# Optimization experiments

Hardware: AMD Instinct MI355X
Metric: run time of the kernel (lower is better)

## Reference

```python
import jax, jax.numpy as jnp
import numpy as np

N = 50000      # nodes (single ntype 'author')
E = 800000     # edges per relation (avg degree 16)
IN = 256       # in_size
H = 4          # num_heads
D = 64         # out_size per head
NEG_SLOPE = 0.2  # DGL GATConv default LeakyReLU slope


def setup_inputs() -> dict:
    key = jax.random.key(0)
    ks = jax.random.split(key, 16)
    s = 1.0 / np.sqrt(IN)
    inp = {
        "h":   jax.random.normal(ks[0], (N, IN), jnp.float32),
        "Wg1": jax.random.normal(ks[1], (H * D, IN), jnp.float32) * s,
        "al1": jax.random.normal(ks[2], (H, D), jnp.float32) * s,
        "ar1": jax.random.normal(ks[3], (H, D), jnp.float32) * s,
        "b1":  jax.random.normal(ks[4], (H * D,), jnp.float32) * 0.01,
        "Wg2": jax.random.normal(ks[5], (H * D, IN), jnp.float32) * s,
        "al2": jax.random.normal(ks[6], (H, D), jnp.float32) * s,
        "ar2": jax.random.normal(ks[7], (H, D), jnp.float32) * s,
        "b2":  jax.random.normal(ks[8], (H * D,), jnp.float32) * 0.01,
        "Wfc": jax.random.normal(ks[9], (H * D, 2 * H * D), jnp.float32) * (1.0 / np.sqrt(2 * H * D)),
        "bfc": jax.random.normal(ks[10], (H * D,), jnp.float32) * 0.01,
        "src1": jax.random.randint(ks[11], (E,), 0, N, jnp.int32),
        "dst1": jax.random.randint(ks[12], (E,), 0, N, jnp.int32),
        "src2": jax.random.randint(ks[13], (E,), 0, N, jnp.int32),
        "dst2": jax.random.randint(ks[14], (E,), 0, N, jnp.int32),
    }
    return inp


def _gat(h, W, al, ar, b, src, dst):
    # DGL GATConv: linear proj -> per-head attn logits -> edge softmax over dst -> scatter-sum
    feat = (h @ W.T).reshape(N, H, D)                       # [N,H,D]
    el = jnp.sum(feat * al, axis=-1)                        # [N,H]
    er = jnp.sum(feat * ar, axis=-1)                        # [N,H]
    e = jax.nn.leaky_relu(el[src] + er[dst], NEG_SLOPE)     # [E,H]
    emax = jax.ops.segment_max(e, dst, num_segments=N)      # [N,H]
    ex = jnp.exp(e - emax[dst])                             # [E,H]
    denom = jax.ops.segment_sum(ex, dst, num_segments=N)    # [N,H]
    alpha = ex / denom[dst]                                 # [E,H]
    msg = feat[src] * alpha[..., None]                      # [E,H,D]
    out = jax.ops.segment_sum(msg, dst, num_segments=N)     # [N,H,D]
    return out.reshape(N, H * D) + b                        # flatten(1) + bias


def reference(h, Wg1, al1, ar1, b1, Wg2, al2, ar2, b2, Wfc, bfc,
              src1, dst1, src2, dst2):
    o1 = _gat(h, Wg1, al1, ar1, b1, src1, dst1)             # metapath 1
    o2 = _gat(h, Wg2, al2, ar2, b2, src2, dst2)             # metapath 2
    sem = jnp.concatenate([o1, o2], axis=1)                 # [N, 2*H*D]
    return sem @ Wfc.T + bfc                                # [N, H*D]
```

## Files before the change

kernel.cpp:

```cpp
#include <hip/hip_runtime.h>
#include <hip/hip_bf16.h>
#include <cfloat>

#define NN 50000
#define EE 800000
#define CAP 64

typedef short bf16x8 __attribute__((ext_vector_type(8)));
typedef float f32x4 __attribute__((ext_vector_type(4)));

__device__ __forceinline__ float leaky(float x) { return x > 0.f ? x : 0.2f * x; }

__device__ __forceinline__ ushort f2b(float x) {
  union { float f; uint u; } v; v.f = x;
  uint r = (v.u + 0x7fffu + ((v.u >> 16) & 1u)) >> 16;
  return (ushort)r;
}
__device__ __forceinline__ float b2f(ushort u) {
  union { uint u; float f; } v; v.u = ((uint)u) << 16; return v.f;
}

#define NH4   (NN * 256 / 4)
#define NW14  (256 * 256 / 4)
#define NW24  (256 * 256 / 4)
#define NWF4  (256 * 512 / 4)
#define NC4   (2 * NN / 4)
#define B0 NH4
#define B1 (B0 + NW14)
#define B2 (B1 + NW24)
#define B3 (B2 + NWF4)
#define B4 (B3 + NC4)

__global__ __launch_bounds__(256) void fused_prep(const float* __restrict__ h,
                                                  const float* __restrict__ Wg1,
                                                  const float* __restrict__ Wg2,
                                                  const float* __restrict__ Wfc,
                                                  ushort* __restrict__ hb,
                                                  ushort* __restrict__ wg1b,
                                                  ushort* __restrict__ wg2b,
                                                  ushort* __restrict__ wfcb,
                                                  int* __restrict__ cursor) {
  int idx = blockIdx.x * blockDim.x + threadIdx.x;
  const float* in;
  ushort* outp;
  int off;
  if (idx < B0) { in = h; outp = hb; off = idx; }
  else if (idx < B1) { in = Wg1; outp = wg1b; off = idx - B0; }
  else if (idx < B2) { in = Wg2; outp = wg2b; off = idx - B1; }
  else if (idx < B3) { in = Wfc; outp = wfcb; off = idx - B2; }
  else if (idx < B4) {
    int4 z = make_int4(0, 0, 0, 0);
    *(int4*)(cursor + (idx - B3) * 4) = z;
    return;
  } else return;
  float4 v = *(const float4*)(in + (size_t)off * 4);
  ushort4 o;
  o.x = f2b(v.x); o.y = f2b(v.y); o.z = f2b(v.z); o.w = f2b(v.w);
  *(ushort4*)(outp + (size_t)off * 4) = o;
}

#define NPROJX ((NN + 127) / 128)
#define PROJ_BLOCKS (NPROJX * 2 * 2)
#define SCAT_BLOCKS (2 * EE / 8 / 256 + 1)
#define MERGED_GRID (SCAT_BLOCKS * 3)

__global__ __launch_bounds__(256) void proj_scatter(const ushort* __restrict__ A,
                                                    const ushort* __restrict__ B1w,
                                                    const ushort* __restrict__ B2w,
                                                    ushort* __restrict__ C, int M,
                                                    const int* __restrict__ src1,
                                                    const int* __restrict__ dst1,
                                                    const int* __restrict__ src2,
                                                    const int* __restrict__ dst2,
                                                    int* __restrict__ cursor,
                                                    ushort* __restrict__ esrc) {
  int r3 = blockIdx.x % 3;
  int g3 = blockIdx.x / 3;
  if (r3 == 0) {
    int g = g3 * 256 + threadIdx.x;
    const int EG = EE / 8;
    if (g >= 2 * EG) return;
    const int* src;
    const int* dst;
    int off, nodeoff;
    if (g < EG) { src = src1; dst = dst1; off = g * 8; nodeoff = 0; }
    else { src = src2; dst = dst2; off = (g - EG) * 8; nodeoff = NN; }
    int4 da = *(const int4*)(dst + off);
    int4 db = *(const int4*)(dst + off + 4);
    int4 sa = *(const int4*)(src + off);
    int4 sb = *(const int4*)(src + off + 4);
    int n0 = nodeoff + da.x, n1 = nodeoff + da.y, n2 = nodeoff + da.z, n3 = nodeoff + da.w;
    int n4 = nodeoff + db.x, n5 = nodeoff + db.y, n6 = nodeoff + db.z, n7 = nodeoff + db.w;
    int p0 = atomicAdd(&cursor[n0], 1);
    int p1 = atomicAdd(&cursor[n1], 1);
    int p2 = atomicAdd(&cursor[n2], 1);
    int p3 = atomicAdd(&cursor[n3], 1);
    int p4 = atomicAdd(&cursor[n4], 1);
    int p5 = atomicAdd(&cursor[n5], 1);
    int p6 = atomicAdd(&cursor[n6], 1);
    int p7 = atomicAdd(&cursor[n7], 1);
    if (p0 < CAP) esrc[(size_t)n0 * CAP + p0] = (ushort)sa.x;
    if (p1 < CAP) esrc[(size_t)n1 * CAP + p1] = (ushort)sa.y;
    if (p2 < CAP) esrc[(size_t)n2 * CAP + p2] = (ushort)sa.z;
    if (p3 < CAP) esrc[(size_t)n3 * CAP + p3] = (ushort)sa.w;
    if (p4 < CAP) esrc[(size_t)n4 * CAP + p4] = (ushort)sb.x;
    if (p5 < CAP) esrc[(size_t)n5 * CAP + p5] = (ushort)sb.y;
    if (p6 < CAP) esrc[(size_t)n6 * CAP + p6] = (ushort)sb.z;
    if (p7 < CAP) esrc[(size_t)n7 * CAP + p7] = (ushort)sb.w;
    return;
  }
  __shared__ __align__(16) ushort As[128][40];
  __shared__ __align__(16) ushort Bs[128][40];
  int pb = 2 * g3 + (r3 - 1);
  if (pb >= PROJ_BLOCKS) return;
  int bz = pb / (NPROJX * 2);
  int rem = pb - bz * (NPROJX * 2);
  int by = rem / NPROJX;
  int bx = rem - by * NPROJX;
  const ushort* B = bz ? B2w : B1w;
  ushort* Cz = C + (size_t)bz * NN * 256;
  int t = threadIdx.x;
  int wave = t >> 6, lane = t & 63;
  int m0 = bx * 128, n0 = by * 128;
  int wm = (wave >> 1) * 64, wn = (wave & 1) * 64;
  int quad = lane >> 4, l15 = lane & 15;
  f32x4 acc[4][4] = {};
  for (int k0 = 0; k0 < 256; k0 += 32) {
#pragma unroll
    for (int i = 0; i < 2; ++i) {
      int c = t + 256 * i;
      int row = c >> 2, ko = (c & 3) * 8;
      uint4 av = make_uint4(0u, 0u, 0u, 0u);
      int gr = m0 + row;
      if (gr < M) av = *(const uint4*)(A + (size_t)gr * 256 + k0 + ko);
      *(uint4*)&As[row][ko] = av;
      uint4 bv = *(const uint4*)(B + (size_t)(n0 + row) * 256 + k0 + ko);
      *(uint4*)&Bs[row][ko] = bv;
    }
    __syncthreads();
    bf16x8 af[4], bf[4];
#pragma unroll
    for (int mt = 0; mt < 4; ++mt) af[mt] = *(const bf16x8*)&As[wm + mt * 16 + l15][quad * 8];
#pragma unroll
    for (int nt = 0; nt < 4; ++nt) bf[nt] = *(const bf16x8*)&Bs[wn + nt * 16 + l15][quad * 8];
#pragma unroll
    for (int mt = 0; mt < 4; ++mt)
#pragma unroll
      for (int nt = 0; nt < 4; ++nt)
        acc[mt][nt] = __builtin_amdgcn_mfma_f32_16x16x32_bf16(af[mt], bf[nt], acc[mt][nt], 0, 0, 0);
    __syncthreads();
  }
#pragma unroll
  for (int mt = 0; mt < 4; ++mt)
#pragma unroll
    for (int r = 0; r < 4; ++r) {
      int row = m0 + wm + mt * 16 + quad * 4 + r;
      if (row < M) {
#pragma unroll
        for (int nt = 0; nt < 4; ++nt)
          Cz[(size_t)row * 256 + n0 + wn + nt * 16 + l15] = f2b(acc[mt][nt][r]);
      }
    }
}

__global__ __launch_bounds__(256) void mfma_fc(const ushort* __restrict__ A0,
                                               const ushort* __restrict__ A1,
                                               const ushort* __restrict__ B,
                                               const float* __restrict__ bias,
                                               float* __restrict__ C, int M) {
  __shared__ __align__(16) ushort As[128][40];
  __shared__ __align__(16) ushort Bs[128][40];
  int t = threadIdx.x;
  int wave = t >> 6, lane = t & 63;
  int m0 = blockIdx.x * 128, n0 = blockIdx.y * 128;
  int wm = (wave >> 1) * 64, wn = (wave & 1) * 64;
  int quad = lane >> 4, l15 = lane & 15;
  f32x4 acc[4][4] = {};
  for (int k0 = 0; k0 < 512; k0 += 32) {
    const ushort* Asrc = (k0 < 256) ? A0 : A1;
    int ka = k0 & 255;
#pragma unroll
    for (int i = 0; i < 2; ++i) {
      int c = t + 256 * i;
      int row = c >> 2, ko = (c & 3) * 8;
      uint4 av = make_uint4(0u, 0u, 0u, 0u);
      int gr = m0 + row;
      if (gr < M) av = *(const uint4*)(Asrc + (size_t)gr * 256 + ka + ko);
      *(uint4*)&As[row][ko] = av;
      uint4 bv = *(const uint4*)(B + (size_t)(n0 + row) * 512 + k0 + ko);
      *(uint4*)&Bs[row][ko] = bv;
    }
    __syncthreads();
    bf16x8 af[4], bf[4];
#pragma unroll
    for (int mt = 0; mt < 4; ++mt) af[mt] = *(const bf16x8*)&As[wm + mt * 16 + l15][quad * 8];
#pragma unroll
    for (int nt = 0; nt < 4; ++nt) bf[nt] = *(const bf16x8*)&Bs[wn + nt * 16 + l15][quad * 8];
#pragma unroll
    for (int mt = 0; mt < 4; ++mt)
#pragma unroll
      for (int nt = 0; nt < 4; ++nt)
        acc[mt][nt] = __builtin_amdgcn_mfma_f32_16x16x32_bf16(af[mt], bf[nt], acc[mt][nt], 0, 0, 0);
    __syncthreads();
  }
#pragma unroll
  for (int mt = 0; mt < 4; ++mt)
#pragma unroll
    for (int r = 0; r < 4; ++r) {
      int row = m0 + wm + mt * 16 + quad * 4 + r;
      if (row < M) {
#pragma unroll
        for (int nt = 0; nt < 4; ++nt) {
          int col = n0 + wn + nt * 16 + l15;
          C[(size_t)row * 256 + col] = acc[mt][nt][r] + bias[col];
        }
      }
    }
}

__global__ __launch_bounds__(256) void eler_kernel(const ushort* __restrict__ feat,
                                                   const float* __restrict__ al1,
                                                   const float* __restrict__ ar1,
                                                   const float* __restrict__ al2,
                                                   const float* __restrict__ ar2,
                                                   float* __restrict__ el,
                                                   float* __restrict__ er) {
  int n = blockIdx.x, c = threadIdx.x;
  const float* al = (n < NN) ? al1 : al2;
  const float* ar = (n < NN) ? ar1 : ar2;
  float v = b2f(feat[(size_t)n * 256 + c]);
  float pl = v * al[c], pr = v * ar[c];
#pragma unroll
  for (int o = 32; o > 0; o >>= 1) {
    pl += __shfl_xor(pl, o);
    pr += __shfl_xor(pr, o);
  }
  if ((c & 63) == 0) {
    el[n * 4 + (c >> 6)] = pl;
    er[n * 4 + (c >> 6)] = pr;
  }
}

__global__ __launch_bounds__(256) void gat_accum(const ushort* __restrict__ feat,
                                                 const float* __restrict__ el,
                                                 const float* __restrict__ er,
                                                 const ushort* __restrict__ esrc,
                                                 const int* __restrict__ deg,
                                                 const float* __restrict__ b1,
                                                 const float* __restrict__ b2,
                                                 ushort* __restrict__ o1,
                                                 ushort* __restrict__ o2) {
  int n = blockIdx.x * 4 + (threadIdx.x >> 6);
  if (n >= 2 * NN) return;
  int lane = threadIdx.x & 63;
  int h = lane >> 4;
  int d = min(deg[n], CAP);
  int nodeoff = (n < NN) ? 0 : NN;
  const ushort* lst = esrc + (size_t)n * CAP;
  float erh = er[n * 4 + h];
  float dsum = 0.f;
  float4 acc0 = make_float4(0.f, 0.f, 0.f, 0.f);
  float4 acc1 = make_float4(0.f, 0.f, 0.f, 0.f);
  float4 acc2 = make_float4(0.f, 0.f, 0.f, 0.f);
  float4 acc3 = make_float4(0.f, 0.f, 0.f, 0.f);
  int i = 0;
  for (; i + 4 <= d; i += 4) {
    ushort4 ss = *(const ushort4*)(lst + i);
    int s0 = ss.x + nodeoff, s1 = ss.y + nodeoff, s2 = ss.z + nodeoff, s3 = ss.w + nodeoff;
    ushort4 f0 = *(const ushort4*)(feat + (size_t)s0 * 256 + lane * 4);
    ushort4 f1 = *(const ushort4*)(feat + (size_t)s1 * 256 + lane * 4);
    ushort4 f2 = *(const ushort4*)(feat + (size_t)s2 * 256 + lane * 4);
    ushort4 f3 = *(const ushort4*)(feat + (size_t)s3 * 256 + lane * 4);
    float x0 = __expf(leaky(el[s0 * 4 + h] + erh));
    float x1 = __expf(leaky(el[s1 * 4 + h] + erh));
    float x2 = __expf(leaky(el[s2 * 4 + h] + erh));
    float x3 = __expf(leaky(el[s3 * 4 + h] + erh));
    dsum += (x0 + x1) + (x2 + x3);
    acc0.x += x0 * b2f(f0.x); acc0.y += x0 * b2f(f0.y);
    acc0.z += x0 * b2f(f0.z); acc0.w += x0 * b2f(f0.w);
    acc1.x += x1 * b2f(f1.x); acc1.y += x1 * b2f(f1.y);
    acc1.z += x1 * b2f(f1.z); acc1.w += x1 * b2f(f1.w);
    acc2.x += x2 * b2f(f2.x); acc2.y += x2 * b2f(f2.y);
    acc2.z += x2 * b2f(f2.z); acc2.w += x2 * b2f(f2.w);
    acc3.x += x3 * b2f(f3.x); acc3.y += x3 * b2f(f3.y);
    acc3.z += x3 * b2f(f3.z); acc3.w += x3 * b2f(f3.w);
  }
  for (; i < d; ++i) {
    int s0 = lst[i] + nodeoff;
    float x0 = __expf(leaky(el[s0 * 4 + h] + erh));
    ushort4 f0 = *(const ushort4*)(feat + (size_t)s0 * 256 + lane * 4);
    dsum += x0;
    acc0.x += x0 * b2f(f0.x); acc0.y += x0 * b2f(f0.y);
    acc0.z += x0 * b2f(f0.z); acc0.w += x0 * b2f(f0.w);
  }
  float inv = (d > 0) ? 1.f / dsum : 0.f;
  const float* bias = (n < NN) ? b1 : b2;
  ushort* outp = (n < NN) ? (o1 + (size_t)n * 256) : (o2 + (size_t)(n - NN) * 256);
  float4 bv = *(const float4*)(bias + lane * 4);
  ushort4 ov;
  ov.x = f2b(((acc0.x + acc1.x) + (acc2.x + acc3.x)) * inv + bv.x);
  ov.y = f2b(((acc0.y + acc1.y) + (acc2.y + acc3.y)) * inv + bv.y);
  ov.z = f2b(((acc0.z + acc1.z) + (acc2.z + acc3.z)) * inv + bv.z);
  ov.w = f2b(((acc0.w + acc1.w) + (acc2.w + acc3.w)) * inv + bv.w);
  *(ushort4*)(outp + lane * 4) = ov;
}

extern "C" void kernel_launch(void* const* d_in, const int* in_sizes, int n_in,
                              void* d_out, int out_size, void* d_ws, size_t ws_size,
                              hipStream_t stream) {
  const float* h   = (const float*)d_in[0];
  const float* Wg1 = (const float*)d_in[1];
  const float* al1 = (const float*)d_in[2];
  const float* ar1 = (const float*)d_in[3];
  const float* b1  = (const float*)d_in[4];
  const float* Wg2 = (const float*)d_in[5];
  const float* al2 = (const float*)d_in[6];
  const float* ar2 = (const float*)d_in[7];
  const float* b2  = (const float*)d_in[8];
  const float* Wfc = (const float*)d_in[9];
  const float* bfc = (const float*)d_in[10];
  const int* src1  = (const int*)d_in[11];
  const int* dst1  = (const int*)d_in[12];
  const int* src2  = (const int*)d_in[13];
  const int* dst2  = (const int*)d_in[14];
  float* out = (float*)d_out;

  const int N = NN;
  const int N2 = 2 * N;
  char* ws = (char*)d_ws;
  size_t pos = 0;
  auto alloc = [&](size_t bytes) -> void* {
    void* p = ws + pos;
    pos += (bytes + 255) & ~(size_t)255;
    return p;
  };
  ushort* featb = (ushort*)alloc((size_t)N2 * 256 * 2);
  ushort* hb    = (ushort*)alloc((size_t)N * 256 * 2);
  ushort* o2b   = (ushort*)alloc((size_t)N * 256 * 2);
  ushort* wg1b  = (ushort*)alloc((size_t)256 * 256 * 2);
  ushort* wg2b  = (ushort*)alloc((size_t)256 * 256 * 2);
  ushort* wfcb  = (ushort*)alloc((size_t)256 * 512 * 2);
  float* el     = (float*)alloc((size_t)N2 * 4 * 4);
  float* er     = (float*)alloc((size_t)N2 * 4 * 4);
  int* cursor   = (int*)alloc((size_t)N2 * 4);
  ushort* esrc  = (ushort*)alloc((size_t)N2 * CAP * 2);
  ushort* o1b = hb;

  fused_prep<<<(B4 + 255) / 256, 256, 0, stream>>>(h, Wg1, Wg2, Wfc, hb, wg1b, wg2b, wfcb, cursor);

  proj_scatter<<<MERGED_GRID, 256, 0, stream>>>(
      hb, wg1b, wg2b, featb, N, src1, dst1, src2, dst2, cursor, esrc);

  eler_kernel<<<N2, 256, 0, stream>>>(featb, al1, ar1, al2, ar2, el, er);

  gat_accum<<<(N2 + 3) / 4, 256, 0, stream>>>(featb, el, er, esrc, cursor, b1, b2, o1b, o2b);

  mfma_fc<<<dim3((N + 127) / 128, 2), 256, 0, stream>>>(o1b, o2b, wfcb, bfc, out, N);
}
```

Measured before the change: 435.3 us.

## Fuse attention logits into projection epilogue and widen gather loads in aggregation

Computes el/er dot products directly from the MFMA accumulators in the projection kernel epilogue using lane shuffles, eliminating the separate eler kernel and its re-read of the projected features. The aggregation kernel now has each half-wave process alternate edges with 16-byte bf16x8 loads, combining the halves with a shuffle at the end. This trades extra epilogue registers and shuffles in the GEMM for one fewer launch and memory pass, and gives more memory-level parallelism in the gather.

Measured after the change: 382.2 us. 1.14x faster.

```diff
diff --git a/kernel.cpp b/kernel.cpp
--- a/kernel.cpp
+++ b/kernel.cpp
@@ -18,6 +18,12 @@
 }
 __device__ __forceinline__ float b2f(ushort u) {
   union { uint u; float f; } v; v.u = ((uint)u) << 16; return v.f;
+}
+__device__ __forceinline__ float blo(uint u) {
+  union { uint u; float f; } v; v.u = u << 16; return v.f;
+}
+__device__ __forceinline__ float bhi(uint u) {
+  union { uint u; float f; } v; v.u = u & 0xFFFF0000u; return v.f;
 }
 
 #define NH4   (NN * 256 / 4)
@@ -73,7 +79,13 @@
                                                     const int* __restrict__ src2,
                                                     const int* __restrict__ dst2,
                                                     int* __restrict__ cursor,
-                                                    ushort* __restrict__ esrc) {
+                                                    ushort* __restrict__ esrc,
+                                                    const float* __restrict__ al1,
+                                                    const float* __restrict__ ar1,
+                                                    const float* __restrict__ al2,
+                                                    const float* __restrict__ ar2,
+                                                    float* __restrict__ el,
+                                                    float* __restrict__ er) {
   int r3 = blockIdx.x % 3;
   int g3 = blockIdx.x / 3;
   if (r3 == 0) {
@@ -161,6 +173,38 @@
           Cz[(size_t)row * 256 + n0 + wn + nt * 16 + l15] = f2b(acc[mt][nt][r]);
       }
     }
+  const float* alz = bz ? al2 : al1;
+  const float* arz = bz ? ar2 : ar1;
+  int hA = (n0 + wn) >> 6;
+  float a_al[4], a_ar[4];
+#pragma unroll
+  for (int nt = 0; nt < 4; ++nt) {
+    int c = n0 + wn + nt * 16 + l15;
+    a_al[nt] = alz[c];
+    a_ar[nt] = arz[c];
+  }
+#pragma unroll
+  for (int mt = 0; mt < 4; ++mt)
+#pragma unroll
+    for (int r = 0; r < 4; ++r) {
+      float pl = acc[mt][0][r] * a_al[0] + acc[mt][1][r] * a_al[1]
+               + acc[mt][2][r] * a_al[2] + acc[mt][3][r] * a_al[3];
+      float pr = acc[mt][0][r] * a_ar[0] + acc[mt][1][r] * a_ar[1]
+               + acc[mt][2][r] * a_ar[2] + acc[mt][3][r] * a_ar[3];
+#pragma unroll
+      for (int o = 1; o < 16; o <<= 1) {
+        pl += __shfl_xor(pl, o);
+        pr += __shfl_xor(pr, o);
+      }
+      if (l15 == 0) {
+        int row = m0 + wm + mt * 16 + quad * 4 + r;
+        if (row < M) {
+          int gn = bz * NN + row;
+          el[gn * 4 + hA] = pl;
+          er[gn * 4 + hA] = pr;
+        }
+      }
+    }
 }
 
 __global__ __launch_bounds__(256) void mfma_fc(const ushort* __restrict__ A0,
@@ -218,29 +262,6 @@
     }
 }
 
-__global__ __launch_bounds__(256) void eler_kernel(const ushort* __restrict__ feat,
-                                                   const float* __restrict__ al1,
-                                                   const float* __restrict__ ar1,
-                                                   const float* __restrict__ al2,
-                                                   const float* __restrict__ ar2,
-                                                   float* __restrict__ el,
-                                                   float* __restrict__ er) {
-  int n = blockIdx.x, c = threadIdx.x;
-  const float* al = (n < NN) ? al1 : al2;
-  const float* ar = (n < NN) ? ar1 : ar2;
-  float v = b2f(feat[(size_t)n * 256 + c]);
-  float pl = v * al[c], pr = v * ar[c];
-#pragma unroll
-  for (int o = 32; o > 0; o >>= 1) {
-    pl += __shfl_xor(pl, o);
-    pr += __shfl_xor(pr, o);
-  }
-  if ((c & 63) == 0) {
-    el[n * 4 + (c >> 6)] = pl;
-    er[n * 4 + (c >> 6)] = pr;
-  }
-}
-
 __global__ __launch_bounds__(256) void gat_accum(const ushort* __restrict__ feat,
                                                  const float* __restrict__ el,
                                                  const float* __restrict__ er,
@@ -253,56 +274,59 @@
   int n = blockIdx.x * 4 + (threadIdx.x >> 6);
   if (n >= 2 * NN) return;
   int lane = threadIdx.x & 63;
-  int h = lane >> 4;
+  int half = lane >> 5;
+  int l32 = lane & 31;
+  int h = l32 >> 3;
   int d = min(deg[n], CAP);
   int nodeoff = (n < NN) ? 0 : NN;
   const ushort* lst = esrc + (size_t)n * CAP;
   float erh = er[n * 4 + h];
   float dsum = 0.f;
-  float4 acc0 = make_float4(0.f, 0.f, 0.f, 0.f);
-  float4 acc1 = make_float4(0.f, 0.f, 0.f, 0.f);
-  float4 acc2 = make_float4(0.f, 0.f, 0.f, 0.f);
-  float4 acc3 = make_float4(0.f, 0.f, 0.f, 0.f);
-  int i = 0;
-  for (; i + 4 <= d; i += 4) {
-    ushort4 ss = *(const ushort4*)(lst + i);
-    int s0 = ss.x + nodeoff, s1 = ss.y + nodeoff, s2 = ss.z + nodeoff, s3 = ss.w + nodeoff;
-    ushort4 f0 = *(const ushort4*)(feat + (size_t)s0 * 256 + lane * 4);
-    ushort4 f1 = *(const ushort4*)(feat + (size_t)s1 * 256 + lane * 4);
-    ushort4 f2 = *(const ushort4*)(feat + (size_t)s2 * 256 + lane * 4);
-    ushort4 f3 = *(const ushort4*)(feat + (size_t)s3 * 256 + lane * 4);
-    float x0 = __expf(leaky(el[s0 * 4 + h] + erh));
-    float x1 = __expf(leaky(el[s1 * 4 + h] + erh));
-    float x2 = __expf(leaky(el[s2 * 4 + h] + erh));
-    float x3 = __expf(leaky(el[s3 * 4 + h] + erh));
-    dsum += (x0 + x1) + (x2 + x3);
-    acc0.x += x0 * b2f(f0.x); acc0.y += x0 * b2f(f0.y);
-    acc0.z += x0 * b2f(f0.z); acc0.w += x0 * b2f(f0.w);
-    acc1.x += x1 * b2f(f1.x); acc1.y += x1 * b2f(f1.y);
-    acc1.z += x1 * b2f(f1.z); acc1.w += x1 * b2f(f1.w);
-    acc2.x += x2 * b2f(f2.x); acc2.y += x2 * b2f(f2.y);
-    acc2.z += x2 * b2f(f2.z); acc2.w += x2 * b2f(f2.w);
-    acc3.x += x3 * b2f(f3.x); acc3.y += x3 * b2f(f3.y);
-    acc3.z += x3 * b2f(f3.z); acc3.w += x3 * b2f(f3.w);
-  }
-  for (; i < d; ++i) {
-    int s0 = lst[i] + nodeoff;
-    float x0 = __expf(leaky(el[s0 * 4 + h] + erh));
-    ushort4 f0 = *(const ushort4*)(feat + (size_t)s0 * 256 + lane * 4);
-    dsum += x0;
-    acc0.x += x0 * b2f(f0.x); acc0.y += x0 * b2f(f0.y);
-    acc0.z += x0 * b2f(f0.z); acc0.w += x0 * b2f(f0.w);
-  }
-  float inv = (d > 0) ? 1.f / dsum : 0.f;
-  const float* bias = (n < NN) ? b1 : b2;
-  ushort* outp = (n < NN) ? (o1 + (size_t)n * 256) : (o2 + (size_t)(n - NN) * 256);
-  float4 bv = *(const float4*)(bias + lane * 4);
-  ushort4 ov;
-  ov.x = f2b(((acc0.x + acc1.x) + (acc2.x + acc3.x)) * inv + bv.x);
-  ov.y = f2b(((acc0.y + acc1.y) + (acc2.y + acc3.y)) * inv + bv.y);
-  ov.z = f2b(((acc0.z + acc1.z) + (acc2.z + acc3.z)) * inv + bv.z);
-  ov.w = f2b(((acc0.w + acc1.w) + (acc2.w + acc3.w)) * inv + bv.w);
-  *(ushort4*)(outp + lane * 4) = ov;
+  float acc[8] = {0.f, 0.f, 0.f, 0.f, 0.f, 0.f, 0.f, 0.f};
+  int i = half;
+  for (; i + 2 < d; i += 4) {
+    int sA = lst[i] + nodeoff;
+    int sB = lst[i + 2] + nodeoff;
+    uint4 fA = *(const uint4*)(feat + (size_t)sA * 256 + l32 * 8);
+    uint4 fB = *(const uint4*)(feat + (size_t)sB * 256 + l32 * 8);
+    float xA = __expf(leaky(el[sA * 4 + h] + erh));
+    float xB = __expf(leaky(el[sB * 4 + h] + erh));
+    dsum += xA + xB;
+    acc[0] += xA * blo(fA.x); acc[1] += xA * bhi(fA.x);
+    acc[2] += xA * blo(fA.y); acc[3] += xA * bhi(fA.y);
+    acc[4] += xA * blo(fA.z); acc[5] += xA * bhi(fA.z);
+    acc[6] += xA * blo(fA.w); acc[7] += xA * bhi(fA.w);
+    acc[0] += xB * blo(fB.x); acc[1] += xB * bhi(fB.x);
+    acc[2] += xB * blo(fB.y); acc[3] += xB * bhi(fB.y);
+    acc[4] += xB * blo(fB.z); acc[5] += xB * bhi(fB.z);
+    acc[6] += xB * blo(fB.w); acc[7] += xB * bhi(fB.w);
+  }
+  for (; i < d; i += 2) {
+    int sA = lst[i] + nodeoff;
+    uint4 fA = *(const uint4*)(feat + (size_t)sA * 256 + l32 * 8);
+    float xA = __expf(leaky(el[sA * 4 + h] + erh));
+    dsum += xA;
+    acc[0] += xA * blo(fA.x); acc[1] += xA * bhi(fA.x);
+    acc[2] += xA * blo(fA.y); acc[3] += xA * bhi(fA.y);
+    acc[4] += xA * blo(fA.z); acc[5] += xA * bhi(fA.z);
+    acc[6] += xA * blo(fA.w); acc[7] += xA * bhi(fA.w);
+  }
+  dsum += __shfl_xor(dsum, 32);
+#pragma unroll
+  for (int j = 0; j < 8; ++j) acc[j] += __shfl_xor(acc[j], 32);
+  if (half == 0) {
+    float inv = (d > 0) ? 1.f / dsum : 0.f;
+    const float* bias = (n < NN) ? b1 : b2;
+    ushort* outp = (n < NN) ? (o1 + (size_t)n * 256) : (o2 + (size_t)(n - NN) * 256);
+    float4 bv0 = *(const float4*)(bias + l32 * 8);
+    float4 bv1 = *(const float4*)(bias + l32 * 8 + 4);
+    uint4 ov;
+    ov.x = (uint)f2b(acc[0] * inv + bv0.x) | ((uint)f2b(acc[1] * inv + bv0.y) << 16);
+    ov.y = (uint)f2b(acc[2] * inv + bv0.z) | ((uint)f2b(acc[3] * inv + bv0.w) << 16);
+    ov.z = (uint)f2b(acc[4] * inv + bv1.x) | ((uint)f2b(acc[5] * inv + bv1.y) << 16);
+    ov.w = (uint)f2b(acc[6] * inv + bv1.z) | ((uint)f2b(acc[7] * inv + bv1.w) << 16);
+    *(uint4*)(outp + l32 * 8) = ov;
+  }
 }
 
 extern "C" void kernel_launch(void* const* d_in, const int* in_sizes, int n_in,
@@ -349,9 +373,8 @@
   fused_prep<<<(B4 + 255) / 256, 256, 0, stream>>>(h, Wg1, Wg2, Wfc, hb, wg1b, wg2b, wfcb, cursor);
 
   proj_scatter<<<MERGED_GRID, 256, 0, stream>>>(
-      hb, wg1b, wg2b, featb, N, src1, dst1, src2, dst2, cursor, esrc);
-
-  eler_kernel<<<N2, 256, 0, stream>>>(featb, al1, ar1, al2, ar2, el, er);
+      hb, wg1b, wg2b, featb, N, src1, dst1, src2, dst2, cursor, esrc,
+      al1, ar1, al2, ar2, el, er);
 
   gat_accum<<<(N2 + 3) / 4, 256, 0, stream>>>(featb, el, er, esrc, cursor, b1, b2, o1b, o2b);
 
```
